# Kernel optimization log

Measured on AMD Instinct MI355X. Metric: run time of the kernel, lower is better.

The kernel has to match this reference:

```python
import jax, jax.numpy as jnp
import numpy as np

T, H, V = 2048, 2048, 32000
NH, NKV, DH = 16, 4, 128
E, K, I = 16, 2, 1024
EPS = 1e-6
THETA = 1000000.0


def _rms(x, w):
    # RMSNorm with add_unit_offset: scale = (1 + w)
    v = jnp.mean(x * x, axis=-1, keepdims=True)
    return x * jax.lax.rsqrt(v + EPS) * (1.0 + w)


def _rope(x, pos):
    # x: [T, heads, DH], neox-style rotate-half RoPE
    inv = 1.0 / (THETA ** (jnp.arange(0, DH, 2, dtype=jnp.float32) / DH))
    ang = pos.astype(jnp.float32)[:, None] * inv[None, :]  # [T, DH/2]
    c, s = jnp.cos(ang)[:, None, :], jnp.sin(ang)[:, None, :]
    x1, x2 = x[..., : DH // 2], x[..., DH // 2 :]
    return jnp.concatenate([x1 * c - x2 * s, x2 * c + x1 * s], axis=-1)


def setup_inputs():
    key = jax.random.key(0)
    ks = jax.random.split(key, 12)

    def n(k, shp, scale=0.02):
        return jax.random.normal(k, shp, dtype=jnp.float32) * scale

    return {
        "input_ids": jax.random.randint(ks[0], (T,), 0, V),
        "positions": jnp.arange(T),
        "hidden_states": jax.random.normal(ks[1], (T, H), dtype=jnp.float32),
        "spec_step_idx": 0,
        "embed_w": n(ks[2], (V, H)),
        "fc_w": n(ks[3], (2 * H, H)),
        "pre_fc_emb_w": jnp.zeros((H,), jnp.float32),
        "pre_fc_hid_w": jnp.zeros((H,), jnp.float32),
        "in_ln_w": jnp.zeros((H,), jnp.float32),
        "post_ln_w": jnp.zeros((H,), jnp.float32),
        "final_norm_w": jnp.zeros((H,), jnp.float32),
        "wq": n(ks[4], (H, NH * DH)),
        "wk": n(ks[5], (H, NKV * DH)),
        "wv": n(ks[6], (H, NKV * DH)),
        "wo": n(ks[7], (NH * DH, H)),
        "q_norm_w": jnp.zeros((DH,), jnp.float32),
        "k_norm_w": jnp.zeros((DH,), jnp.float32),
        "router_w": n(ks[8], (H, E)),
        "w_gate": n(ks[9], (E, H, I)),
        "w_up": n(ks[10], (E, H, I)),
        "w_down": n(ks[11], (E, I, H)),
    }


def reference(input_ids, positions, hidden_states, spec_step_idx, embed_w, fc_w,
              pre_fc_emb_w, pre_fc_hid_w, in_ln_w, post_ln_w, final_norm_w,
              wq, wk, wv, wo, q_norm_w, k_norm_w, router_w, w_gate, w_up, w_down):
    # 1-3. embed -> pre_fc norms -> concat -> fc (2H -> H, no bias)
    emb = _rms(embed_w[input_ids], pre_fc_emb_w)
    hid = _rms(hidden_states, pre_fc_hid_w)
    x = jnp.concatenate([emb, hid], axis=-1) @ fc_w  # [T, H]

    # 4. decoder layer (layer_idx = spec_step_idx % 1 == 0); vLLM fused add-RMSNorm residual pattern
    residual = x
    x = _rms(x, in_ln_w)

    # GQA attention with per-head q/k RMSNorm + RoPE, causal
    q = _rms((x @ wq).reshape(T, NH, DH), q_norm_w)
    k = _rms((x @ wk).reshape(T, NKV, DH), k_norm_w)
    v = (x @ wv).reshape(T, NKV, DH)
    q, k = _rope(q, positions), _rope(k, positions)
    rep = NH // NKV
    k, v = jnp.repeat(k, rep, axis=1), jnp.repeat(v, rep, axis=1)  # [T, NH, DH]
    scores = jnp.einsum("qhd,khd->hqk", q, k) * (DH ** -0.5)
    causal = positions[:, None] >= positions[None, :]
    scores = jnp.where(causal[None], scores, jnp.float32(-1e30))
    attn = jax.nn.softmax(scores, axis=-1)
    x = jnp.einsum("hqk,khd->qhd", attn, v).reshape(T, NH * DH) @ wo

    # post-attention norm with fused residual add
    x = x + residual
    residual = x
    x = _rms(x, post_ln_w)

    # MoE: softmax router, top-k renormalized, SwiGLU experts (dense weighted combine)
    probs = jax.nn.softmax(x @ router_w, axis=-1)  # [T, E]
    topv, topi = jax.lax.top_k(probs, K)
    topv = topv / jnp.sum(topv, axis=-1, keepdims=True)
    gates = jnp.zeros((T, E), x.dtype).at[jnp.arange(T)[:, None], topi].set(topv)
    g = jnp.einsum("th,ehi->tei", x, w_gate)
    u = jnp.einsum("th,ehi->tei", x, w_up)
    a = jax.nn.silu(g) * u  # [T, E, I]
    x = jnp.einsum("tei,eih,te->th", a, w_down, gates)

    # 5. final norm with residual add
    return _rms(x + residual, final_norm_w)
```

## Files before the change

kernel.cpp:

```cpp
#include <hip/hip_runtime.h>
#include <cstddef>


typedef unsigned short u16b;
typedef __attribute__((ext_vector_type(8))) short s8v;
typedef __attribute__((ext_vector_type(4))) float f4v;

#define T_TOK 2048
#define HID   2048

__device__ __forceinline__ float bf2f(u16b h) {
  return __uint_as_float(((unsigned int)h) << 16);
}
__device__ __forceinline__ u16b f2bf(float f) {
  unsigned int u = __float_as_uint(f);
  return (u16b)((u + 0x7fffu + ((u >> 16) & 1u)) >> 16);
}
__device__ __forceinline__ void split2(float f, u16b& hi, u16b& lo) {
  hi = f2bf(f);
  lo = f2bf(f - bf2f(hi));
}
__device__ __forceinline__ unsigned long long pack4(const u16b* p) {
  return (unsigned long long)p[0] | ((unsigned long long)p[1] << 16) |
         ((unsigned long long)p[2] << 32) | ((unsigned long long)p[3] << 48);
}
__device__ __forceinline__ f4v mfma_b(s8v a, s8v b, f4v c) {
  return __builtin_amdgcn_mfma_f32_16x16x32_bf16(a, b, c, 0, 0, 0);
}
union FragCvt { unsigned long long q[2]; s8v v; };

__device__ __forceinline__ float blk_sum_256(float v, float* lds4) {
  #pragma unroll
  for (int off = 32; off > 0; off >>= 1) v += __shfl_down(v, off);
  int tid = threadIdx.x;
  if ((tid & 63) == 0) lds4[tid >> 6] = v;
  __syncthreads();
  return lds4[0] + lds4[1] + lds4[2] + lds4[3];
}

__global__ void zero_counts_kernel(int* counts) {
  if (threadIdx.x < 16) counts[threadIdx.x] = 0;
}

__global__ __launch_bounds__(256) void embed_cat_kernel(
    const int* __restrict__ ids, const float* __restrict__ embw,
    const float* __restrict__ hid, const float* __restrict__ w_emb,
    const float* __restrict__ w_hid, u16b* __restrict__ catp) {
  __shared__ float lds[4];
  int t = blockIdx.x, which = blockIdx.y, tid = threadIdx.x;
  const float* src;
  const float* w;
  if (which == 0) { src = embw + (size_t)ids[t] * HID; w = w_emb; }
  else            { src = hid  + (size_t)t * HID;      w = w_hid; }
  u16b* dst = catp + (size_t)t * 8192 + which * 2048;
  float v[8]; float ss = 0.f;
  #pragma unroll
  for (int i = 0; i < 8; ++i) { v[i] = src[tid + i * 256]; ss += v[i] * v[i]; }
  float tot = blk_sum_256(ss, lds);
  float scale = rsqrtf(tot * (1.f / (float)HID) + 1e-6f);
  #pragma unroll
  for (int i = 0; i < 8; ++i) {
    int j = tid + i * 256;
    float val = v[i] * scale * (1.f + w[j]);
    u16b h, l;
    split2(val, h, l);
    dst[j] = h;
    dst[4096 + j] = l;
  }
}

__global__ __launch_bounds__(256) void rms_f32_kernel(
    const float* __restrict__ X, const float* __restrict__ W, float* __restrict__ Y) {
  __shared__ float lds[4];
  int t = blockIdx.x, tid = threadIdx.x;
  const float* row = X + (size_t)t * HID;
  float v[8]; float ss = 0.f;
  #pragma unroll
  for (int i = 0; i < 8; ++i) { v[i] = row[tid + i * 256]; ss += v[i] * v[i]; }
  float tot = blk_sum_256(ss, lds);
  float scale = rsqrtf(tot * (1.f / (float)HID) + 1e-6f);
  float* yrow = Y + (size_t)t * HID;
  #pragma unroll
  for (int i = 0; i < 8; ++i) {
    int j = tid + i * 256;
    yrow[j] = v[i] * scale * (1.f + W[j]);
  }
}

__global__ __launch_bounds__(256) void rms_split_kernel(
    const float* __restrict__ X, const float* __restrict__ W, u16b* __restrict__ Yp) {
  __shared__ float lds[4];
  int t = blockIdx.x, tid = threadIdx.x;
  const float* row = X + (size_t)t * HID;
  float v[8]; float ss = 0.f;
  #pragma unroll
  for (int i = 0; i < 8; ++i) { v[i] = row[tid + i * 256]; ss += v[i] * v[i]; }
  float tot = blk_sum_256(ss, lds);
  float scale = rsqrtf(tot * (1.f / (float)HID) + 1e-6f);
  u16b* yrow = Yp + (size_t)t * (2 * HID);
  #pragma unroll
  for (int i = 0; i < 8; ++i) {
    int j = tid + i * 256;
    float val = v[i] * scale * (1.f + W[j]);
    u16b h, l;
    split2(val, h, l);
    yrow[j] = h;
    yrow[HID + j] = l;
  }
}

__global__ __launch_bounds__(256) void tsplit_kernel(
    const float* __restrict__ B, u16b* __restrict__ Bt,
    int Kf, int N, int row_off) {
  __shared__ u16b ht[64][68];
  __shared__ u16b lt[64][68];
  int n0 = blockIdx.x * 64, k0 = blockIdx.y * 64;
  int tid = threadIdx.x;
  int kl = tid >> 4, nl = (tid & 15) * 4;
  #pragma unroll
  for (int p = 0; p < 4; ++p) {
    int kk = p * 16 + kl;
    float4 f = *(const float4*)&B[(size_t)(k0 + kk) * N + n0 + nl];
    float ff[4] = {f.x, f.y, f.z, f.w};
    #pragma unroll
    for (int j = 0; j < 4; ++j) {
      u16b h, l;
      split2(ff[j], h, l);
      ht[nl + j][kk] = h;
      lt[nl + j][kk] = l;
    }
  }
  __syncthreads();
  int ldo = 2 * Kf;
  int nr = tid >> 2, kc = (tid & 3) * 16;
  u16b* orow = Bt + (size_t)(row_off + n0 + nr) * ldo + k0 + kc;
  #pragma unroll
  for (int c = 0; c < 4; ++c) {
    *(unsigned long long*)(orow + c * 4)      = *(const unsigned long long*)&ht[nr][kc + c * 4];
    *(unsigned long long*)(orow + Kf + c * 4) = *(const unsigned long long*)&lt[nr][kc + c * 4];
  }
}

template <int EP>
__global__ __launch_bounds__(256) void gemm_bs(
    const u16b* __restrict__ Ap, const u16b* __restrict__ Bp,
    float* __restrict__ C, const float* __restrict__ addend,
    float* __restrict__ kout, float* __restrict__ vtout,
    int M, int N, int Kf) {
  __shared__ __attribute__((aligned(16))) u16b Ahs[64 * 40];
  __shared__ __attribute__((aligned(16))) u16b Als[64 * 40];
  __shared__ __attribute__((aligned(16))) u16b Bhs[64 * 40];
  __shared__ __attribute__((aligned(16))) u16b Bls[64 * 40];
  int n0 = blockIdx.x * 64, m0 = blockIdx.y * 64;
  int tid = threadIdx.x;
  int wave = tid >> 6, lane = tid & 63;
  int wm = wave >> 1, wn = wave & 1;
  int l16 = lane & 15, quad = lane >> 4;
  int lda = 2 * Kf;
  int sr = tid >> 2, skc = (tid & 3) * 8;
  const u16b* apH = Ap + (size_t)(m0 + sr) * lda + skc;
  const u16b* bpH = Bp + (size_t)(n0 + sr) * lda + skc;
  int sb = sr * 40 + skc;

  f4v acc[2][2];
  #pragma unroll
  for (int i = 0; i < 2; ++i)
    #pragma unroll
    for (int j = 0; j < 2; ++j) acc[i][j] = (f4v)0.0f;

  for (int k0 = 0; k0 < Kf; k0 += 32) {
    s8v ta = *(const s8v*)(apH + k0);
    s8v tb = *(const s8v*)(apH + Kf + k0);
    s8v tc = *(const s8v*)(bpH + k0);
    s8v td = *(const s8v*)(bpH + Kf + k0);
    __syncthreads();
    FragCvt u;
    u.v = ta;
    *(unsigned long long*)&Ahs[sb]     = u.q[0];
    *(unsigned long long*)&Ahs[sb + 4] = u.q[1];
    u.v = tb;
    *(unsigned long long*)&Als[sb]     = u.q[0];
    *(unsigned long long*)&Als[sb + 4] = u.q[1];
    u.v = tc;
    *(unsigned long long*)&Bhs[sb]     = u.q[0];
    *(unsigned long long*)&Bhs[sb + 4] = u.q[1];
    u.v = td;
    *(unsigned long long*)&Bls[sb]     = u.q[0];
    *(unsigned long long*)&Bls[sb + 4] = u.q[1];
    __syncthreads();
    s8v a0  = *(const s8v*)&Ahs[(wm * 32 + l16) * 40 + quad * 8];
    s8v a1  = *(const s8v*)&Ahs[(wm * 32 + 16 + l16) * 40 + quad * 8];
    s8v b0  = *(const s8v*)&Bhs[(wn * 32 + l16) * 40 + quad * 8];
    s8v b1  = *(const s8v*)&Bhs[(wn * 32 + 16 + l16) * 40 + quad * 8];
    s8v a0l = *(const s8v*)&Als[(wm * 32 + l16) * 40 + quad * 8];
    s8v a1l = *(const s8v*)&Als[(wm * 32 + 16 + l16) * 40 + quad * 8];
    s8v b0l = *(const s8v*)&Bls[(wn * 32 + l16) * 40 + quad * 8];
    s8v b1l = *(const s8v*)&Bls[(wn * 32 + 16 + l16) * 40 + quad * 8];
    acc[0][0] = mfma_b(a0, b0, acc[0][0]);
    acc[0][1] = mfma_b(a0, b1, acc[0][1]);
    acc[1][0] = mfma_b(a1, b0, acc[1][0]);
    acc[1][1] = mfma_b(a1, b1, acc[1][1]);
    acc[0][0] = mfma_b(a0, b0l, acc[0][0]);
    acc[0][1] = mfma_b(a0, b1l, acc[0][1]);
    acc[1][0] = mfma_b(a1, b0l, acc[1][0]);
    acc[1][1] = mfma_b(a1, b1l, acc[1][1]);
    acc[0][0] = mfma_b(a0l, b0, acc[0][0]);
    acc[0][1] = mfma_b(a0l, b1, acc[0][1]);
    acc[1][0] = mfma_b(a1l, b0, acc[1][0]);
    acc[1][1] = mfma_b(a1l, b1, acc[1][1]);
  }

  if (EP == 0) {
    #pragma unroll
    for (int i = 0; i < 2; ++i)
      #pragma unroll
      for (int j = 0; j < 2; ++j)
        #pragma unroll
        for (int r = 0; r < 4; ++r) {
          int mrow = m0 + wm * 32 + i * 16 + quad * 4 + r;
          int col = n0 + wn * 32 + j * 16 + l16;
          size_t idx = (size_t)mrow * N + col;
          C[idx] = acc[i][j][r] + (addend ? addend[idx] : 0.0f);
        }
  } else {
    if (n0 < 2048) {
      #pragma unroll
      for (int i = 0; i < 2; ++i)
        #pragma unroll
        for (int j = 0; j < 2; ++j)
          #pragma unroll
          for (int r = 0; r < 4; ++r) {
            int mrow = m0 + wm * 32 + i * 16 + quad * 4 + r;
            int col = n0 + wn * 32 + j * 16 + l16;
            C[(size_t)mrow * 2048 + col] = acc[i][j][r];
          }
    } else if (n0 < 2560) {
      #pragma unroll
      for (int i = 0; i < 2; ++i)
        #pragma unroll
        for (int j = 0; j < 2; ++j)
          #pragma unroll
          for (int r = 0; r < 4; ++r) {
            int mrow = m0 + wm * 32 + i * 16 + quad * 4 + r;
            int col = n0 + wn * 32 + j * 16 + l16 - 2048;
            kout[(size_t)mrow * 512 + col] = acc[i][j][r];
          }
    } else {
      #pragma unroll
      for (int i = 0; i < 2; ++i)
        #pragma unroll
        for (int j = 0; j < 2; ++j) {
          int vrow = n0 + wn * 32 + j * 16 + l16 - 2560;
          int mbase = m0 + wm * 32 + i * 16 + quad * 4;
          float4 vv;
          vv.x = acc[i][j][0]; vv.y = acc[i][j][1];
          vv.z = acc[i][j][2]; vv.w = acc[i][j][3];
          *(float4*)&vtout[(size_t)vrow * 2048 + mbase] = vv;
        }
    }
  }
}

__global__ __launch_bounds__(128) void qknorm_rope_kernel(
    float* __restrict__ X, const float* __restrict__ W,
    const int* __restrict__ positions, int ld) {
  __shared__ float wsum[2];
  __shared__ float xs[128];
  __shared__ float sc;
  int t = blockIdx.x, hh = blockIdx.y, d = threadIdx.x;
  float* row = X + (size_t)t * ld + hh * 128;
  float x = row[d];
  float ss = x * x;
  #pragma unroll
  for (int off = 32; off > 0; off >>= 1) ss += __shfl_down(ss, off);
  if ((d & 63) == 0) wsum[d >> 6] = ss;
  __syncthreads();
  if (d == 0) sc = rsqrtf((wsum[0] + wsum[1]) * (1.f / 128.f) + 1e-6f);
  __syncthreads();
  float xn = x * sc * (1.f + W[d]);
  xs[d] = xn;
  __syncthreads();
  int pos = positions[t];
  int i = d & 63;
  float invf = exp2f((float)i * (-19.931568569324174f / 64.f));
  float ang = (float)pos * invf;
  float cv = cosf(ang), sv = sinf(ang);
  float other = xs[d ^ 64];
  row[d] = (d < 64) ? (xn * cv - other * sv) : (xn * cv + other * sv);
}

template <int MODE>
__global__ __launch_bounds__(256) void gemm_moe(
    const u16b* __restrict__ Ap, int lda,
    const float* __restrict__ B, const float* __restrict__ B2,
    u16b* __restrict__ hout, float* __restrict__ moeout,
    const int* __restrict__ counts, const int* __restrict__ list,
    const float* __restrict__ gatebuf, int N, int K) {
  __shared__ __attribute__((aligned(16))) u16b As[128 * 40];
  __shared__ __attribute__((aligned(16))) u16b Bs[64 * 40];
  __shared__ __attribute__((aligned(16))) u16b B2s[(MODE == 1) ? 64 * 40 : 8];

  int n0 = blockIdx.x * 64;
  int m0 = blockIdx.y * 128;
  int e = blockIdx.z;
  int cnt = counts[e];
  if (m0 >= cnt) return;
  list += e * T_TOK;
  B += (size_t)e * K * N;
  if (MODE == 1) B2 += (size_t)e * K * N;

  int tid = threadIdx.x;
  int wave = tid >> 6, lane = tid & 63;
  int wm = wave >> 1, wn = wave & 1;
  int l16 = lane & 15, quad = lane >> 4;

  int ar = tid >> 1, ac0 = (tid & 1) * 2;
  int axr = (ar >> 3) & 3;
  const u16b* aptr;
  {
    int mr = m0 + ar;
    if (mr > cnt - 1) mr = cnt - 1;
    int entry = list[mr];
    int arow = (MODE == 1) ? (entry >> 1) : entry;
    aptr = Ap + (size_t)arow * lda;
  }
  int bk = tid >> 3, bn8 = (tid & 7) * 8;
  const float* bptr = B + (size_t)bk * N + n0 + bn8;
  const float* b2ptr = nullptr;
  if (MODE == 1) b2ptr = B2 + (size_t)bk * N + n0 + bn8;
  int bcol = (bk >> 3) * 8 + (bk & 7);

  f4v acc[4][2];
  f4v acc2[4][2];
  #pragma unroll
  for (int i = 0; i < 4; ++i)
    #pragma unroll
    for (int j = 0; j < 2; ++j) { acc[i][j] = (f4v)0.0f; acc2[i][j] = (f4v)0.0f; }

  for (int k0 = 0; k0 < K; k0 += 32) {
    s8v ta0 = *(const s8v*)(aptr + k0 + ac0 * 8);
    s8v ta1 = *(const s8v*)(aptr + k0 + ac0 * 8 + 8);
    float4 g0 = *(const float4*)(bptr + (size_t)k0 * N);
    float4 g1 = *(const float4*)(bptr + (size_t)k0 * N + 4);
    float4 h0, h1;
    if (MODE == 1) {
      h0 = *(const float4*)(b2ptr + (size_t)k0 * N);
      h1 = *(const float4*)(b2ptr + (size_t)k0 * N + 4);
    }
    __syncthreads();
    *(s8v*)&As[ar * 40 + ((ac0 ^ axr) * 8)]       = ta0;
    *(s8v*)&As[ar * 40 + (((ac0 + 1) ^ axr) * 8)] = ta1;
    {
      float f[8] = {g0.x, g0.y, g0.z, g0.w, g1.x, g1.y, g1.z, g1.w};
      #pragma unroll
      for (int x = 0; x < 8; ++x) {
        int n = bn8 + x;
        int col = ((bk >> 3) ^ ((n >> 3) & 3)) * 8 + (bk & 7);
        Bs[n * 40 + col] = f2bf(f[x]);
      }
      if (MODE == 1) {
        float f2[8] = {h0.x, h0.y, h0.z, h0.w, h1.x, h1.y, h1.z, h1.w};
        #pragma unroll
        for (int x = 0; x < 8; ++x) {
          int n = bn8 + x;
          int col = ((bk >> 3) ^ ((n >> 3) & 3)) * 8 + (bk & 7);
          B2s[n * 40 + col] = f2bf(f2[x]);
        }
      }
    }
    __syncthreads();
    s8v a[4], b[2], c2[2];
    #pragma unroll
    for (int i = 0; i < 4; ++i) {
      int row = wm * 64 + i * 16 + l16;
      a[i] = *(const s8v*)&As[row * 40 + ((quad ^ ((row >> 3) & 3)) * 8)];
    }
    #pragma unroll
    for (int j = 0; j < 2; ++j) {
      int row = wn * 32 + j * 16 + l16;
      b[j] = *(const s8v*)&Bs[row * 40 + ((quad ^ ((row >> 3) & 3)) * 8)];
      if (MODE == 1)
        c2[j] = *(const s8v*)&B2s[row * 40 + ((quad ^ ((row >> 3) & 3)) * 8)];
    }
    __builtin_amdgcn_s_setprio(1);
    #pragma unroll
    for (int i = 0; i < 4; ++i)
      #pragma unroll
      for (int j = 0; j < 2; ++j) {
        acc[i][j] = mfma_b(a[i], b[j], acc[i][j]);
        if (MODE == 1) acc2[i][j] = mfma_b(a[i], c2[j], acc2[i][j]);
      }
    __builtin_amdgcn_s_setprio(0);
  }

  #pragma unroll
  for (int i = 0; i < 4; ++i)
    #pragma unroll
    for (int j = 0; j < 2; ++j)
      #pragma unroll
      for (int r = 0; r < 4; ++r) {
        int mrow = m0 + wm * 64 + i * 16 + quad * 4 + r;
        if (mrow < cnt) {
          int slot = list[mrow];
          int col = n0 + wn * 32 + j * 16 + l16;
          if (MODE == 1) {
            float g = acc[i][j][r], u = acc2[i][j][r];
            float hv = g / (1.0f + __expf(-g)) * u;
            hout[(size_t)slot * N + col] = f2bf(hv);
          } else {
            moeout[(size_t)slot * N + col] = acc[i][j][r] * gatebuf[slot];
          }
        }
      }
}

__global__ __launch_bounds__(256) void flash_kernel(
    const float* __restrict__ Q, const float* __restrict__ Kb,
    const float* __restrict__ VbT, u16b* __restrict__ attnp) {
  __shared__ __attribute__((aligned(16))) u16b Khi[32 * 136];
  __shared__ __attribute__((aligned(16))) u16b Klo[32 * 136];
  __shared__ __attribute__((aligned(16))) u16b Vthi[128 * 40];
  __shared__ __attribute__((aligned(16))) u16b Vtlo[128 * 40];
  __shared__ float Ss[32 * 36];
  __shared__ __attribute__((aligned(16))) u16b Phi[32 * 40];
  __shared__ __attribute__((aligned(16))) u16b Plo[32 * 40];
  __shared__ float red[32 * 8];
  __shared__ float mrow[32], lrow[32], arow[32];

  int qt = (gridDim.x - 1) - blockIdx.x;
  int h = blockIdx.y;
  int g = h >> 2;
  int tid = threadIdx.x;
  int wave = tid >> 6, lane = tid & 63;
  int l16 = lane & 15, quad = lane >> 4;
  int sm = wave >> 1, sn = wave & 1;

  s8v qhi[4], qlo[4];
  {
    const float* qp = Q + (size_t)(qt * 32 + sm * 16 + l16) * 2048 + h * 128 + quad * 8;
    #pragma unroll
    for (int kc = 0; kc < 4; ++kc) {
      float4 f0 = *(const float4*)(qp + kc * 32);
      float4 f1 = *(const float4*)(qp + kc * 32 + 4);
      float f[8] = {f0.x, f0.y, f0.z, f0.w, f1.x, f1.y, f1.z, f1.w};
      u16b hi[8], lo[8];
      #pragma unroll
      for (int x = 0; x < 8; ++x) split2(f[x], hi[x], lo[x]);
      FragCvt ch, cl;
      ch.q[0] = pack4(hi); ch.q[1] = pack4(hi + 4);
      cl.q[0] = pack4(lo); cl.q[1] = pack4(lo + 4);
      qhi[kc] = ch.v; qlo[kc] = cl.v;
    }
  }

  if (tid < 32) { mrow[tid] = -1e30f; lrow[tid] = 0.f; }

  f4v o[4];
  #pragma unroll
  for (int db = 0; db < 4; ++db) o[db] = (f4v)0.0f;

  int krow = tid >> 3, ksk = (tid & 7) * 16;
  int vd = tid >> 1, vk0 = (tid & 1) * 16;
  int sr = tid >> 3, sp = tid & 7;

  const u16b* krow_h = &Khi[(sn * 16 + l16) * 136];
  const u16b* krow_l = &Klo[(sn * 16 + l16) * 136];

  for (int kt = 0; kt <= qt; ++kt) {
    __syncthreads();
    {
      const float* ks = Kb + (size_t)(kt * 32 + krow) * 512 + g * 128 + ksk;
      int kb = krow * 136 + ksk;
      #pragma unroll
      for (int half = 0; half < 2; ++half) {
        float4 f0 = *(const float4*)(ks + half * 8);
        float4 f1 = *(const float4*)(ks + half * 8 + 4);
        float f[8] = {f0.x, f0.y, f0.z, f0.w, f1.x, f1.y, f1.z, f1.w};
        u16b hi[8], lo[8];
        #pragma unroll
        for (int x = 0; x < 8; ++x) split2(f[x], hi[x], lo[x]);
        *(unsigned long long*)&Khi[kb + half * 8]     = pack4(hi);
        *(unsigned long long*)&Khi[kb + half * 8 + 4] = pack4(hi + 4);
        *(unsigned long long*)&Klo[kb + half * 8]     = pack4(lo);
        *(unsigned long long*)&Klo[kb + half * 8 + 4] = pack4(lo + 4);
      }
      const float* vs = VbT + (size_t)(g * 128 + vd) * 2048 + kt * 32 + vk0;
      int vb = vd * 40 + vk0;
      #pragma unroll
      for (int half = 0; half < 2; ++half) {
        float4 f0 = *(const float4*)(vs + half * 8);
        float4 f1 = *(const float4*)(vs + half * 8 + 4);
        float f[8] = {f0.x, f0.y, f0.z, f0.w, f1.x, f1.y, f1.z, f1.w};
        u16b hi[8], lo[8];
        #pragma unroll
        for (int x = 0; x < 8; ++x) split2(f[x], hi[x], lo[x]);
        *(unsigned long long*)&Vthi[vb + half * 8]     = pack4(hi);
        *(unsigned long long*)&Vthi[vb + half * 8 + 4] = pack4(hi + 4);
        *(unsigned long long*)&Vtlo[vb + half * 8]     = pack4(lo);
        *(unsigned long long*)&Vtlo[vb + half * 8 + 4] = pack4(lo + 4);
      }
    }
    __syncthreads();
    f4v a0 = (f4v)0.0f, a1 = (f4v)0.0f, a2 = (f4v)0.0f;
    __builtin_amdgcn_s_setprio(1);
    #pragma unroll
    for (int kc = 0; kc < 4; ++kc) {
      s8v kh = *(const s8v*)(krow_h + kc * 32 + quad * 8);
      s8v kl = *(const s8v*)(krow_l + kc * 32 + quad * 8);
      a0 = mfma_b(qhi[kc], kh, a0);
      a1 = mfma_b(qhi[kc], kl, a1);
      a2 = mfma_b(qlo[kc], kh, a2);
    }
    __builtin_amdgcn_s_setprio(0);
    {
      f4v sacc = a0 + a1 + a2;
      const float sc = 0.08838834764831845f;
      #pragma unroll
      for (int r = 0; r < 4; ++r) {
        int row_l = sm * 16 + quad * 4 + r;
        int col_l = sn * 16 + l16;
        int qb = qt * 32 + row_l, kb2 = kt * 32 + col_l;
        Ss[row_l * 36 + col_l] = (kb2 <= qb) ? sacc[r] * sc : -1e30f;
      }
    }
    __syncthreads();
    float mx = -3e38f;
    #pragma unroll
    for (int c = sp * 4; c < sp * 4 + 4; ++c) mx = fmaxf(mx, Ss[sr * 36 + c]);
    red[sr * 8 + sp] = mx;
    __syncthreads();
    if (sp == 0) {
      float mn = mrow[sr];
      #pragma unroll
      for (int p = 0; p < 8; ++p) mn = fmaxf(mn, red[sr * 8 + p]);
      arow[sr] = __expf(mrow[sr] - mn);
      mrow[sr] = mn;
    }
    __syncthreads();
    {
      float m = mrow[sr];
      float sum = 0.f;
      #pragma unroll
      for (int c = sp * 4; c < sp * 4 + 4; ++c) {
        float e2 = __expf(Ss[sr * 36 + c] - m);
        u16b eh, el;
        split2(e2, eh, el);
        Phi[sr * 40 + c] = eh;
        Plo[sr * 40 + c] = el;
        sum += e2;
      }
      red[sr * 8 + sp] = sum;
    }
    __syncthreads();
    if (sp == 0) {
      float s2 = 0.f;
      #pragma unroll
      for (int p = 0; p < 8; ++p) s2 += red[sr * 8 + p];
      lrow[sr] = lrow[sr] * arow[sr] + s2;
    }
    {
      f4v arv;
      arv[0] = arow[sm * 16 + quad * 4 + 0];
      arv[1] = arow[sm * 16 + quad * 4 + 1];
      arv[2] = arow[sm * 16 + quad * 4 + 2];
      arv[3] = arow[sm * 16 + quad * 4 + 3];
      #pragma unroll
      for (int db = 0; db < 4; ++db) o[db] *= arv;

      s8v pah = *(const s8v*)&Phi[(sm * 16 + l16) * 40 + quad * 8];
      s8v pal = *(const s8v*)&Plo[(sm * 16 + l16) * 40 + quad * 8];
      __builtin_amdgcn_s_setprio(1);
      #pragma unroll
      for (int db = 0; db < 4; ++db) {
        int vrow = sn * 64 + db * 16 + l16;
        s8v vh = *(const s8v*)&Vthi[vrow * 40 + quad * 8];
        s8v vl = *(const s8v*)&Vtlo[vrow * 40 + quad * 8];
        o[db] = mfma_b(pah, vh, o[db]);
        o[db] = mfma_b(pah, vl, o[db]);
        o[db] = mfma_b(pal, vh, o[db]);
      }
      __builtin_amdgcn_s_setprio(0);
    }
  }
  __syncthreads();
  {
    int row0 = sm * 16 + quad * 4;
    f4v invv;
    invv[0] = 1.f / lrow[row0 + 0];
    invv[1] = 1.f / lrow[row0 + 1];
    invv[2] = 1.f / lrow[row0 + 2];
    invv[3] = 1.f / lrow[row0 + 3];
    #pragma unroll
    for (int db = 0; db < 4; ++db) o[db] *= invv;
    #pragma unroll
    for (int r = 0; r < 4; ++r) {
      u16b* ob = attnp + (size_t)(qt * 32 + row0 + r) * 4096 + h * 128 + sn * 64 + l16;
      #pragma unroll
      for (int db = 0; db < 4; ++db) {
        u16b hh, ll;
        split2(o[db][r], hh, ll);
        ob[db * 16] = hh;
        ob[2048 + db * 16] = ll;
      }
    }
  }
}

__global__ __launch_bounds__(256) void router_kernel(
    const float* __restrict__ xn2, const float* __restrict__ rw,
    int* __restrict__ counts, int* __restrict__ list, float* __restrict__ gatebuf) {
  __shared__ float red[256];
  __shared__ float logits[16];
  int t = blockIdx.x, tid = threadIdx.x;
  int e = tid >> 4, p = tid & 15;
  const float* xr = xn2 + (size_t)t * HID;
  float s = 0.f;
  for (int j = p * 128; j < p * 128 + 128; ++j) s += xr[j] * rw[j * 16 + e];
  red[tid] = s;
  __syncthreads();
  if (tid < 16) {
    float l = 0.f;
    #pragma unroll
    for (int p2 = 0; p2 < 16; ++p2) l += red[tid * 16 + p2];
    logits[tid] = l;
  }
  __syncthreads();
  if (tid == 0) {
    int i0 = 0; float l0 = logits[0];
    for (int i = 1; i < 16; ++i) if (logits[i] > l0) { l0 = logits[i]; i0 = i; }
    int i1 = -1; float l1 = -3e38f;
    for (int i = 0; i < 16; ++i) if (i != i0 && logits[i] > l1) { l1 = logits[i]; i1 = i; }
    float g0 = 1.f / (1.f + __expf(l1 - l0));
    float g1 = 1.f - g0;
    int s0 = atomicAdd(&counts[i0], 1);
    list[i0 * T_TOK + s0] = t * 2;
    gatebuf[t * 2] = g0;
    int s1 = atomicAdd(&counts[i1], 1);
    list[i1 * T_TOK + s1] = t * 2 + 1;
    gatebuf[t * 2 + 1] = g1;
  }
}

__global__ __launch_bounds__(256) void final_kernel(
    const float* __restrict__ moeout, const float* __restrict__ resid,
    const float* __restrict__ W, float* __restrict__ out) {
  __shared__ float lds[4];
  int t = blockIdx.x, tid = threadIdx.x;
  const float* m0 = moeout + (size_t)(2 * t) * HID;
  const float* m1 = moeout + (size_t)(2 * t + 1) * HID;
  const float* rr = resid + (size_t)t * HID;
  float v[8]; float ss = 0.f;
  #pragma unroll
  for (int i = 0; i < 8; ++i) {
    int j = tid + i * 256;
    v[i] = m0[j] + m1[j] + rr[j];
    ss += v[i] * v[i];
  }
  float tot = blk_sum_256(ss, lds);
  float scale = rsqrtf(tot * (1.f / (float)HID) + 1e-6f);
  float* orow = out + (size_t)t * HID;
  #pragma unroll
  for (int i = 0; i < 8; ++i) {
    int j = tid + i * 256;
    orow[j] = v[i] * scale * (1.f + W[j]);
  }
}

extern "C" void kernel_launch(void* const* d_in, const int* in_sizes, int n_in,
                              void* d_out, int out_size, void* d_ws, size_t ws_size,
                              hipStream_t stream) {
  const int* input_ids   = (const int*)d_in[0];
  const int* positions   = (const int*)d_in[1];
  const float* hidden    = (const float*)d_in[2];
  const float* embed_w   = (const float*)d_in[4];
  const float* fc_w      = (const float*)d_in[5];
  const float* pre_emb   = (const float*)d_in[6];
  const float* pre_hid   = (const float*)d_in[7];
  const float* in_ln     = (const float*)d_in[8];
  const float* post_ln   = (const float*)d_in[9];
  const float* final_w   = (const float*)d_in[10];
  const float* wq        = (const float*)d_in[11];
  const float* wk        = (const float*)d_in[12];
  const float* wv        = (const float*)d_in[13];
  const float* wo        = (const float*)d_in[14];
  const float* qnw       = (const float*)d_in[15];
  const float* knw       = (const float*)d_in[16];
  const float* rw        = (const float*)d_in[17];
  const float* wg        = (const float*)d_in[18];
  const float* wu        = (const float*)d_in[19];
  const float* wd        = (const float*)d_in[20];

  char* ws = (char*)d_ws;
  u16b*  catp   = (u16b*)(ws + 0);
  u16b*  qkvw   = (u16b*)(ws + 0);
  float* moeout = (float*)(ws + 0);
  float* x      = (float*)(ws + 33554432);
  u16b*  xnp    = (u16b*)(ws + 50331648);
  u16b*  wotw   = (u16b*)(ws + 50331648);
  float* q      = (float*)(ws + 67108864);
  u16b*  hbuf16 = (u16b*)(ws + 67108864);
  float* kbuf   = (float*)(ws + 83886080);
  float* vbufT  = (float*)(ws + 88080384);
  u16b*  fctw   = (u16b*)(ws + 92274688);
  u16b*  attnp  = (u16b*)(ws + 92274688);
  float* x2     = (float*)(ws + 109051904);
  float* xn2    = (float*)(ws + 125829120);
  int*   counts = (int*)(ws + 142606336);
  int*   list   = (int*)(ws + 142606592);
  float* gateb  = (float*)(ws + 142737664);

  zero_counts_kernel<<<1, 64, 0, stream>>>(counts);
  embed_cat_kernel<<<dim3(2048, 2), 256, 0, stream>>>(input_ids, embed_w, hidden,
                                                      pre_emb, pre_hid, catp);
  tsplit_kernel<<<dim3(32, 64), 256, 0, stream>>>(fc_w, fctw, 4096, 2048, 0);
  gemm_bs<0><<<dim3(32, 32), 256, 0, stream>>>(catp, fctw, x, nullptr,
                                               nullptr, nullptr, 2048, 2048, 4096);
  tsplit_kernel<<<dim3(32, 32), 256, 0, stream>>>(wq, qkvw, 2048, 2048, 0);
  tsplit_kernel<<<dim3(8, 32), 256, 0, stream>>>(wk, qkvw, 2048, 512, 2048);
  tsplit_kernel<<<dim3(8, 32), 256, 0, stream>>>(wv, qkvw, 2048, 512, 2560);
  rms_split_kernel<<<2048, 256, 0, stream>>>(x, in_ln, xnp);
  gemm_bs<1><<<dim3(48, 32), 256, 0, stream>>>(xnp, qkvw, q, nullptr,
                                               kbuf, vbufT, 2048, 3072, 2048);
  tsplit_kernel<<<dim3(32, 32), 256, 0, stream>>>(wo, wotw, 2048, 2048, 0);
  qknorm_rope_kernel<<<dim3(2048, 16), 128, 0, stream>>>(q, qnw, positions, 2048);
  qknorm_rope_kernel<<<dim3(2048, 4), 128, 0, stream>>>(kbuf, knw, positions, 512);
  flash_kernel<<<dim3(64, 16), 256, 0, stream>>>(q, kbuf, vbufT, attnp);
  gemm_bs<0><<<dim3(32, 32), 256, 0, stream>>>(attnp, wotw, x2, x,
                                               nullptr, nullptr, 2048, 2048, 2048);
  rms_f32_kernel<<<2048, 256, 0, stream>>>(x2, post_ln, xn2);
  rms_split_kernel<<<2048, 256, 0, stream>>>(x2, post_ln, xnp);
  router_kernel<<<2048, 256, 0, stream>>>(xn2, rw, counts, list, gateb);
  gemm_moe<1><<<dim3(16, 16, 16), 256, 0, stream>>>(xnp, 4096, wg, wu, hbuf16,
                                                    nullptr, counts, list, nullptr,
                                                    1024, 2048);
  gemm_moe<2><<<dim3(32, 16, 16), 256, 0, stream>>>(hbuf16, 1024, wd, nullptr, nullptr,
                                                    moeout, counts, list, gateb,
                                                    2048, 1024);
  final_kernel<<<2048, 256, 0, stream>>>(moeout, x2, final_w, (float*)d_out);
}
```

Measured before the change: 1.541 ms.

## Enlarge dense GEMM M-tile and pre-split K/V to bf16 pairs before attention

The split-bf16 dense GEMM now computes a 128x64 tile per block instead of 64x64, with wider vector LDS stores and raised wave priority around the MFMA block. The block count is halved and each B tile is reused across more rows. The QKV GEMM epilogue writes V transposed as hi/lo bf16 pairs, and a new K norm+RoPE kernel writes K as hi/lo bf16, so the flash kernel loads pre-split data instead of converting fp32 on every tile. The cost is more registers per thread and lower grid occupancy for the GEMMs.

```diff
diff --git a/kernel.cpp b/kernel.cpp
--- a/kernel.cpp
+++ b/kernel.cpp
@@ -145,79 +145,79 @@
 __global__ __launch_bounds__(256) void gemm_bs(
     const u16b* __restrict__ Ap, const u16b* __restrict__ Bp,
     float* __restrict__ C, const float* __restrict__ addend,
-    float* __restrict__ kout, float* __restrict__ vtout,
+    float* __restrict__ kout, u16b* __restrict__ vtout,
     int M, int N, int Kf) {
-  __shared__ __attribute__((aligned(16))) u16b Ahs[64 * 40];
-  __shared__ __attribute__((aligned(16))) u16b Als[64 * 40];
+  __shared__ __attribute__((aligned(16))) u16b Ahs[128 * 40];
+  __shared__ __attribute__((aligned(16))) u16b Als[128 * 40];
   __shared__ __attribute__((aligned(16))) u16b Bhs[64 * 40];
   __shared__ __attribute__((aligned(16))) u16b Bls[64 * 40];
-  int n0 = blockIdx.x * 64, m0 = blockIdx.y * 64;
+  int n0 = blockIdx.x * 64, m0 = blockIdx.y * 128;
   int tid = threadIdx.x;
   int wave = tid >> 6, lane = tid & 63;
   int wm = wave >> 1, wn = wave & 1;
   int l16 = lane & 15, quad = lane >> 4;
   int lda = 2 * Kf;
-  int sr = tid >> 2, skc = (tid & 3) * 8;
-  const u16b* apH = Ap + (size_t)(m0 + sr) * lda + skc;
-  const u16b* bpH = Bp + (size_t)(n0 + sr) * lda + skc;
-  int sb = sr * 40 + skc;
-
-  f4v acc[2][2];
-  #pragma unroll
-  for (int i = 0; i < 2; ++i)
+  int ar = tid >> 1, ac = (tid & 1) * 16;
+  int br = tid >> 2, bc = (tid & 3) * 8;
+  const u16b* apH = Ap + (size_t)(m0 + ar) * lda + ac;
+  const u16b* bpH = Bp + (size_t)(n0 + br) * lda + bc;
+  int sa = ar * 40 + ac;
+  int sbb = br * 40 + bc;
+
+  f4v acc[4][2];
+  #pragma unroll
+  for (int i = 0; i < 4; ++i)
     #pragma unroll
     for (int j = 0; j < 2; ++j) acc[i][j] = (f4v)0.0f;
 
   for (int k0 = 0; k0 < Kf; k0 += 32) {
-    s8v ta = *(const s8v*)(apH + k0);
-    s8v tb = *(const s8v*)(apH + Kf + k0);
-    s8v tc = *(const s8v*)(bpH + k0);
-    s8v td = *(const s8v*)(bpH + Kf + k0);
-    __syncthreads();
-    FragCvt u;
-    u.v = ta;
-    *(unsigned long long*)&Ahs[sb]     = u.q[0];
-    *(unsigned long long*)&Ahs[sb + 4] = u.q[1];
-    u.v = tb;
-    *(unsigned long long*)&Als[sb]     = u.q[0];
-    *(unsigned long long*)&Als[sb + 4] = u.q[1];
-    u.v = tc;
-    *(unsigned long long*)&Bhs[sb]     = u.q[0];
-    *(unsigned long long*)&Bhs[sb + 4] = u.q[1];
-    u.v = td;
-    *(unsigned long long*)&Bls[sb]     = u.q[0];
-    *(unsigned long long*)&Bls[sb + 4] = u.q[1];
-    __syncthreads();
-    s8v a0  = *(const s8v*)&Ahs[(wm * 32 + l16) * 40 + quad * 8];
-    s8v a1  = *(const s8v*)&Ahs[(wm * 32 + 16 + l16) * 40 + quad * 8];
-    s8v b0  = *(const s8v*)&Bhs[(wn * 32 + l16) * 40 + quad * 8];
-    s8v b1  = *(const s8v*)&Bhs[(wn * 32 + 16 + l16) * 40 + quad * 8];
-    s8v a0l = *(const s8v*)&Als[(wm * 32 + l16) * 40 + quad * 8];
-    s8v a1l = *(const s8v*)&Als[(wm * 32 + 16 + l16) * 40 + quad * 8];
-    s8v b0l = *(const s8v*)&Bls[(wn * 32 + l16) * 40 + quad * 8];
-    s8v b1l = *(const s8v*)&Bls[(wn * 32 + 16 + l16) * 40 + quad * 8];
-    acc[0][0] = mfma_b(a0, b0, acc[0][0]);
-    acc[0][1] = mfma_b(a0, b1, acc[0][1]);
-    acc[1][0] = mfma_b(a1, b0, acc[1][0]);
-    acc[1][1] = mfma_b(a1, b1, acc[1][1]);
-    acc[0][0] = mfma_b(a0, b0l, acc[0][0]);
-    acc[0][1] = mfma_b(a0, b1l, acc[0][1]);
-    acc[1][0] = mfma_b(a1, b0l, acc[1][0]);
-    acc[1][1] = mfma_b(a1, b1l, acc[1][1]);
-    acc[0][0] = mfma_b(a0l, b0, acc[0][0]);
-    acc[0][1] = mfma_b(a0l, b1, acc[0][1]);
-    acc[1][0] = mfma_b(a1l, b0, acc[1][0]);
-    acc[1][1] = mfma_b(a1l, b1, acc[1][1]);
+    s8v ah0 = *(const s8v*)(apH + k0);
+    s8v ah1 = *(const s8v*)(apH + k0 + 8);
+    s8v al0 = *(const s8v*)(apH + Kf + k0);
+    s8v al1 = *(const s8v*)(apH + Kf + k0 + 8);
+    s8v bh  = *(const s8v*)(bpH + k0);
+    s8v bl  = *(const s8v*)(bpH + Kf + k0);
+    __syncthreads();
+    *(s8v*)&Ahs[sa]     = ah0;
+    *(s8v*)&Ahs[sa + 8] = ah1;
+    *(s8v*)&Als[sa]     = al0;
+    *(s8v*)&Als[sa + 8] = al1;
+    *(s8v*)&Bhs[sbb] = bh;
+    *(s8v*)&Bls[sbb] = bl;
+    __syncthreads();
+    s8v a[4], al[4], b[2], bl2[2];
+    #pragma unroll
+    for (int i = 0; i < 4; ++i) {
+      int row = wm * 64 + i * 16 + l16;
+      a[i]  = *(const s8v*)&Ahs[row * 40 + quad * 8];
+      al[i] = *(const s8v*)&Als[row * 40 + quad * 8];
+    }
+    #pragma unroll
+    for (int j = 0; j < 2; ++j) {
+      int row = wn * 32 + j * 16 + l16;
+      b[j]   = *(const s8v*)&Bhs[row * 40 + quad * 8];
+      bl2[j] = *(const s8v*)&Bls[row * 40 + quad * 8];
+    }
+    __builtin_amdgcn_s_setprio(1);
+    #pragma unroll
+    for (int i = 0; i < 4; ++i)
+      #pragma unroll
+      for (int j = 0; j < 2; ++j) {
+        acc[i][j] = mfma_b(a[i], b[j], acc[i][j]);
+        acc[i][j] = mfma_b(a[i], bl2[j], acc[i][j]);
+        acc[i][j] = mfma_b(al[i], b[j], acc[i][j]);
+      }
+    __builtin_amdgcn_s_setprio(0);
   }
 
   if (EP == 0) {
     #pragma unroll
-    for (int i = 0; i < 2; ++i)
+    for (int i = 0; i < 4; ++i)
       #pragma unroll
       for (int j = 0; j < 2; ++j)
         #pragma unroll
         for (int r = 0; r < 4; ++r) {
-          int mrow = m0 + wm * 32 + i * 16 + quad * 4 + r;
+          int mrow = m0 + wm * 64 + i * 16 + quad * 4 + r;
           int col = n0 + wn * 32 + j * 16 + l16;
           size_t idx = (size_t)mrow * N + col;
           C[idx] = acc[i][j][r] + (addend ? addend[idx] : 0.0f);
@@ -225,37 +225,38 @@
   } else {
     if (n0 < 2048) {
       #pragma unroll
-      for (int i = 0; i < 2; ++i)
+      for (int i = 0; i < 4; ++i)
         #pragma unroll
         for (int j = 0; j < 2; ++j)
           #pragma unroll
           for (int r = 0; r < 4; ++r) {
-            int mrow = m0 + wm * 32 + i * 16 + quad * 4 + r;
+            int mrow = m0 + wm * 64 + i * 16 + quad * 4 + r;
             int col = n0 + wn * 32 + j * 16 + l16;
             C[(size_t)mrow * 2048 + col] = acc[i][j][r];
           }
     } else if (n0 < 2560) {
       #pragma unroll
-      for (int i = 0; i < 2; ++i)
+      for (int i = 0; i < 4; ++i)
         #pragma unroll
         for (int j = 0; j < 2; ++j)
           #pragma unroll
           for (int r = 0; r < 4; ++r) {
-            int mrow = m0 + wm * 32 + i * 16 + quad * 4 + r;
+            int mrow = m0 + wm * 64 + i * 16 + quad * 4 + r;
             int col = n0 + wn * 32 + j * 16 + l16 - 2048;
             kout[(size_t)mrow * 512 + col] = acc[i][j][r];
           }
     } else {
       #pragma unroll
-      for (int i = 0; i < 2; ++i)
+      for (int i = 0; i < 4; ++i)
         #pragma unroll
         for (int j = 0; j < 2; ++j) {
           int vrow = n0 + wn * 32 + j * 16 + l16 - 2560;
-          int mbase = m0 + wm * 32 + i * 16 + quad * 4;
-          float4 vv;
-          vv.x = acc[i][j][0]; vv.y = acc[i][j][1];
-          vv.z = acc[i][j][2]; vv.w = acc[i][j][3];
-          *(float4*)&vtout[(size_t)vrow * 2048 + mbase] = vv;
+          int mbase = m0 + wm * 64 + i * 16 + quad * 4;
+          u16b hi4[4], lo4[4];
+          #pragma unroll
+          for (int r = 0; r < 4; ++r) split2(acc[i][j][r], hi4[r], lo4[r]);
+          *(unsigned long long*)&vtout[(size_t)vrow * 4096 + mbase]        = pack4(hi4);
+          *(unsigned long long*)&vtout[(size_t)vrow * 4096 + 2048 + mbase] = pack4(lo4);
         }
     }
   }
@@ -289,6 +290,38 @@
   row[d] = (d < 64) ? (xn * cv - other * sv) : (xn * cv + other * sv);
 }
 
+__global__ __launch_bounds__(128) void knorm_rope_split_kernel(
+    const float* __restrict__ X, const float* __restrict__ W,
+    const int* __restrict__ positions, u16b* __restrict__ Kp) {
+  __shared__ float wsum[2];
+  __shared__ float xs[128];
+  __shared__ float sc;
+  int t = blockIdx.x, hh = blockIdx.y, d = threadIdx.x;
+  const float* row = X + (size_t)t * 512 + hh * 128;
+  float x = row[d];
+  float ss = x * x;
+  #pragma unroll
+  for (int off = 32; off > 0; off >>= 1) ss += __shfl_down(ss, off);
+  if ((d & 63) == 0) wsum[d >> 6] = ss;
+  __syncthreads();
+  if (d == 0) sc = rsqrtf((wsum[0] + wsum[1]) * (1.f / 128.f) + 1e-6f);
+  __syncthreads();
+  float xn = x * sc * (1.f + W[d]);
+  xs[d] = xn;
+  __syncthreads();
+  int pos = positions[t];
+  int i = d & 63;
+  float invf = exp2f((float)i * (-19.931568569324174f / 64.f));
+  float ang = (float)pos * invf;
+  float cv = cosf(ang), sv = sinf(ang);
+  float other = xs[d ^ 64];
+  float val = (d < 64) ? (xn * cv - other * sv) : (xn * cv + other * sv);
+  u16b h, l;
+  split2(val, h, l);
+  Kp[(size_t)t * 1024 + hh * 128 + d] = h;
+  Kp[(size_t)t * 1024 + 512 + hh * 128 + d] = l;
+}
+
 template <int MODE>
 __global__ __launch_bounds__(256) void gemm_moe(
     const u16b* __restrict__ Ap, int lda,
@@ -328,7 +361,6 @@
   const float* bptr = B + (size_t)bk * N + n0 + bn8;
   const float* b2ptr = nullptr;
   if (MODE == 1) b2ptr = B2 + (size_t)bk * N + n0 + bn8;
-  int bcol = (bk >> 3) * 8 + (bk & 7);
 
   f4v acc[4][2];
   f4v acc2[4][2];
@@ -415,8 +447,8 @@
 }
 
 __global__ __launch_bounds__(256) void flash_kernel(
-    const float* __restrict__ Q, const float* __restrict__ Kb,
-    const float* __restrict__ VbT, u16b* __restrict__ attnp) {
+    const float* __restrict__ Q, const u16b* __restrict__ Kp,
+    const u16b* __restrict__ Vtp, u16b* __restrict__ attnp) {
   __shared__ __attribute__((aligned(16))) u16b Khi[32 * 136];
   __shared__ __attribute__((aligned(16))) u16b Klo[32 * 136];
   __shared__ __attribute__((aligned(16))) u16b Vthi[128 * 40];
@@ -467,38 +499,28 @@
   const u16b* krow_l = &Klo[(sn * 16 + l16) * 136];
 
   for (int kt = 0; kt <= qt; ++kt) {
+    const u16b* ksh = Kp + (size_t)(kt * 32 + krow) * 1024 + g * 128 + ksk;
+    s8v kh0 = *(const s8v*)(ksh);
+    s8v kh1 = *(const s8v*)(ksh + 8);
+    s8v kl0 = *(const s8v*)(ksh + 512);
+    s8v kl1 = *(const s8v*)(ksh + 520);
+    const u16b* vsh = Vtp + (size_t)(g * 128 + vd) * 4096 + kt * 32 + vk0;
+    s8v vh0 = *(const s8v*)(vsh);
+    s8v vh1 = *(const s8v*)(vsh + 8);
+    s8v vl0 = *(const s8v*)(vsh + 2048);
+    s8v vl1 = *(const s8v*)(vsh + 2056);
     __syncthreads();
     {
-      const float* ks = Kb + (size_t)(kt * 32 + krow) * 512 + g * 128 + ksk;
       int kb = krow * 136 + ksk;
-      #pragma unroll
-      for (int half = 0; half < 2; ++half) {
-        float4 f0 = *(const float4*)(ks + half * 8);
-        float4 f1 = *(const float4*)(ks + half * 8 + 4);
-        float f[8] = {f0.x, f0.y, f0.z, f0.w, f1.x, f1.y, f1.z, f1.w};
-        u16b hi[8], lo[8];
-        #pragma unroll
-        for (int x = 0; x < 8; ++x) split2(f[x], hi[x], lo[x]);
-        *(unsigned long long*)&Khi[kb + half * 8]     = pack4(hi);
-        *(unsigned long long*)&Khi[kb + half * 8 + 4] = pack4(hi + 4);
-        *(unsigned long long*)&Klo[kb + half * 8]     = pack4(lo);
-        *(unsigned long long*)&Klo[kb + half * 8 + 4] = pack4(lo + 4);
-      }
-      const float* vs = VbT + (size_t)(g * 128 + vd) * 2048 + kt * 32 + vk0;
+      *(s8v*)&Khi[kb]     = kh0;
+      *(s8v*)&Khi[kb + 8] = kh1;
+      *(s8v*)&Klo[kb]     = kl0;
+      *(s8v*)&Klo[kb + 8] = kl1;
       int vb = vd * 40 + vk0;
-      #pragma unroll
-      for (int half = 0; half < 2; ++half) {
-        float4 f0 = *(const float4*)(vs + half * 8);
-        float4 f1 = *(const float4*)(vs + half * 8 + 4);
-        float f[8] = {f0.x, f0.y, f0.z, f0.w, f1.x, f1.y, f1.z, f1.w};
-        u16b hi[8], lo[8];
-        #pragma unroll
-        for (int x = 0; x < 8; ++x) split2(f[x], hi[x], lo[x]);
-        *(unsigned long long*)&Vthi[vb + half * 8]     = pack4(hi);
-        *(unsigned long long*)&Vthi[vb + half * 8 + 4] = pack4(hi + 4);
-        *(unsigned long long*)&Vtlo[vb + half * 8]     = pack4(lo);
-        *(unsigned long long*)&Vtlo[vb + half * 8 + 4] = pack4(lo + 4);
-      }
+      *(s8v*)&Vthi[vb]     = vh0;
+      *(s8v*)&Vthi[vb + 8] = vh1;
+      *(s8v*)&Vtlo[vb]     = vl0;
+      *(s8v*)&Vtlo[vb + 8] = vl1;
     }
     __syncthreads();
     f4v a0 = (f4v)0.0f, a1 = (f4v)0.0f, a2 = (f4v)0.0f;
@@ -694,13 +716,14 @@
   u16b*  catp   = (u16b*)(ws + 0);
   u16b*  qkvw   = (u16b*)(ws + 0);
   float* moeout = (float*)(ws + 0);
+  u16b*  vtp    = (u16b*)(ws + 25165824);
   float* x      = (float*)(ws + 33554432);
   u16b*  xnp    = (u16b*)(ws + 50331648);
   u16b*  wotw   = (u16b*)(ws + 50331648);
   float* q      = (float*)(ws + 67108864);
   u16b*  hbuf16 = (u16b*)(ws + 67108864);
   float* kbuf   = (float*)(ws + 83886080);
-  float* vbufT  = (float*)(ws + 88080384);
+  u16b*  kp     = (u16b*)(ws + 88080384);
   u16b*  fctw   = (u16b*)(ws + 92274688);
   u16b*  attnp  = (u16b*)(ws + 92274688);
   float* x2     = (float*)(ws + 109051904);
@@ -713,19 +736,19 @@
   embed_cat_kernel<<<dim3(2048, 2), 256, 0, stream>>>(input_ids, embed_w, hidden,
                                                       pre_emb, pre_hid, catp);
   tsplit_kernel<<<dim3(32, 64), 256, 0, stream>>>(fc_w, fctw, 4096, 2048, 0);
-  gemm_bs<0><<<dim3(32, 32), 256, 0, stream>>>(catp, fctw, x, nullptr,
+  gemm_bs<0><<<dim3(32, 16), 256, 0, stream>>>(catp, fctw, x, nullptr,
                                                nullptr, nullptr, 2048, 2048, 4096);
   tsplit_kernel<<<dim3(32, 32), 256, 0, stream>>>(wq, qkvw, 2048, 2048, 0);
   tsplit_kernel<<<dim3(8, 32), 256, 0, stream>>>(wk, qkvw, 2048, 512, 2048);
   tsplit_kernel<<<dim3(8, 32), 256, 0, stream>>>(wv, qkvw, 2048, 512, 2560);
   rms_split_kernel<<<2048, 256, 0, stream>>>(x, in_ln, xnp);
-  gemm_bs<1><<<dim3(48, 32), 256, 0, stream>>>(xnp, qkvw, q, nullptr,
-                                               kbuf, vbufT, 2048, 3072, 2048);
+  gemm_bs<1><<<dim3(48, 16), 256, 0, stream>>>(xnp, qkvw, q, nullptr,
+                                               kbuf, vtp, 2048, 3072, 2048);
   tsplit_kernel<<<dim3(32, 32), 256, 0, stream>>>(wo, wotw, 2048, 2048, 0);
   qknorm_rope_kernel<<<dim3(2048, 16), 128, 0, stream>>>(q, qnw, positions, 2048);
-  qknorm_rope_kernel<<<dim3(2048, 4), 128, 0, stream>>>(kbuf, knw, positions, 512);
-  flash_kernel<<<dim3(64, 16), 256, 0, stream>>>(q, kbuf, vbufT, attnp);
-  gemm_bs<0><<<dim3(32, 32), 256, 0, stream>>>(attnp, wotw, x2, x,
+  knorm_rope_split_kernel<<<dim3(2048, 4), 128, 0, stream>>>(kbuf, knw, positions, kp);
+  flash_kernel<<<dim3(64, 16), 256, 0, stream>>>(q, kp, vtp, attnp);
+  gemm_bs<0><<<dim3(32, 16), 256, 0, stream>>>(attnp, wotw, x2, x,
                                                nullptr, nullptr, 2048, 2048, 2048);
   rms_f32_kernel<<<2048, 256, 0, stream>>>(x2, post_ln, xn2);
   rms_split_kernel<<<2048, 256, 0, stream>>>(x2, post_ln, xnp);
```

After: 1.482 ms. 1.04x faster.
